# Kernel tuning notes

Hardware: AMD Instinct MI355X
Metric: run time of the kernel (lower is better)

## Reference

```python
import jax, jax.numpy as jnp
import numpy as np

DIM, HEADS, DIM_HEAD = 1024, 16, 64
DIM_INNER = HEADS * DIM_HEAD  # 1024
SCALE = DIM_HEAD ** -0.5


def _rope(t):
    # t: [b, h, n, d]; interleaved-pair RoPE (lucidrains rotary-embedding-torch default)
    d = t.shape[-1]
    n = t.shape[-2]
    inv_freq = 1.0 / (10000.0 ** (jnp.arange(0, d, 2, dtype=jnp.float32) / d))
    angles = jnp.arange(n, dtype=jnp.float32)[:, None] * inv_freq[None, :]  # [n, d/2]
    cos, sin = jnp.cos(angles), jnp.sin(angles)
    t1, t2 = t[..., 0::2], t[..., 1::2]
    r1 = t1 * cos - t2 * sin
    r2 = t1 * sin + t2 * cos
    return jnp.stack([r1, r2], axis=-1).reshape(t.shape)


def setup_inputs() -> dict:
    key = jax.random.key(0)
    ks = jax.random.split(key, 8)
    b, n = 2, 2048
    inp = {
        "x": jax.random.normal(ks[0], (b, n, DIM), dtype=jnp.float32),
        "value_residual": jax.random.normal(ks[1], (b, HEADS, n, DIM_HEAD), dtype=jnp.float32),
        "gamma": jnp.ones((DIM,), dtype=jnp.float32),
        "w_qkv": jax.random.normal(ks[2], (DIM, 3 * DIM_INNER), dtype=jnp.float32) * (DIM ** -0.5),
        "w_mix": jax.random.normal(ks[3], (DIM, HEADS), dtype=jnp.float32) * (DIM ** -0.5),
        "b_mix": jnp.zeros((HEADS,), dtype=jnp.float32),
        "w_gates": jax.random.normal(ks[4], (DIM, HEADS), dtype=jnp.float32) * (DIM ** -0.5),
        "b_gates": jnp.zeros((HEADS,), dtype=jnp.float32),
        "w_out": jax.random.normal(ks[5], (DIM_INNER, DIM), dtype=jnp.float32) * (DIM_INNER ** -0.5),
    }
    return inp


def reference(x, value_residual, gamma, w_qkv, w_mix, b_mix, w_gates, b_gates, w_out):
    b, n, _ = x.shape
    # RMSNorm (lucidrains style: F.normalize * sqrt(dim) * gamma)
    norm = jnp.sqrt(jnp.sum(x * x, axis=-1, keepdims=True))
    xn = x / jnp.maximum(norm, 1e-12) * (DIM ** 0.5) * gamma

    qkv = xn @ w_qkv  # [b, n, 3*h*d]
    qkv = qkv.reshape(b, n, 3, HEADS, DIM_HEAD)
    q, k, v = [jnp.transpose(qkv[:, :, i], (0, 2, 1, 3)) for i in range(3)]  # [b,h,n,d]
    original_values = v

    # learned value-residual lerp
    mix = jax.nn.sigmoid(xn @ w_mix + b_mix)            # [b, n, h]
    mix = jnp.transpose(mix, (0, 2, 1))[..., None]       # [b, h, n, 1]
    v = v * (1.0 - mix) + value_residual * mix

    # rotary on q, k
    q = _rope(q)
    k = _rope(k)

    scores = jnp.einsum("bhid,bhjd->bhij", q, k) * SCALE
    attn = jax.nn.softmax(scores, axis=-1)
    out = jnp.einsum("bhij,bhjd->bhid", attn, v)         # [b, h, n, d]

    gates = jax.nn.sigmoid(xn @ w_gates + b_gates)       # [b, n, h]
    out = out * jnp.transpose(gates, (0, 2, 1))[..., None]

    out = jnp.transpose(out, (0, 2, 1, 3)).reshape(b, n, DIM_INNER)
    return out @ w_out, original_values
```

## Files before the change

### kernel.cpp

```cpp
#include <hip/hip_runtime.h>
#include <hip/hip_bf16.h>
#include <math.h>

#define DIMSZ 1024
#define HEADS 16
#define DHEAD 64
#define NSEQ  2048
#define BATCH 2
#define ROWS  (BATCH*NSEQ)
#define SCALE 0.125f
#define LOG2E 1.4426950408889634f

typedef __attribute__((ext_vector_type(8))) short short8;
typedef __attribute__((ext_vector_type(4))) float floatx4;
typedef __attribute__((ext_vector_type(16))) float floatx16;
typedef __attribute__((ext_vector_type(4))) unsigned uintx4;

#define MFMA16(a,b,c) __builtin_amdgcn_mfma_f32_16x16x32_bf16(a,b,c,0,0,0)
#define MFMA32(a,b,c) __builtin_amdgcn_mfma_f32_32x32x16_bf16(a,b,c,0,0,0)

__device__ __forceinline__ void gl2lds16(const void* g, void* l) {
    __builtin_amdgcn_global_load_lds(
        (const __attribute__((address_space(1))) unsigned int*)g,
        (__attribute__((address_space(3))) unsigned int*)l, 16, 0, 0);
}

__device__ __forceinline__ unsigned short bf16r(float a) {
    unsigned u = __float_as_uint(a);
    u += 0x7fff + ((u >> 16) & 1);
    return (unsigned short)(u >> 16);
}
__device__ __forceinline__ unsigned pack_bf16(float a, float b) {
    unsigned ua = __float_as_uint(a), ub = __float_as_uint(b);
    ua += 0x7fff + ((ua >> 16) & 1);
    ub += 0x7fff + ((ub >> 16) & 1);
    return (ua >> 16) | (ub & 0xffff0000u);
}
__device__ __forceinline__ float2 bf2f(unsigned u) {
    float2 r;
    r.x = __uint_as_float(u << 16);
    r.y = __uint_as_float(u & 0xffff0000u);
    return r;
}
__device__ __forceinline__ unsigned cvtpk(float lo, float hi) {
    unsigned r;
    asm("v_cvt_pk_bf16_f32 %0, %1, %2" : "=v"(r) : "v"(lo), "v"(hi));
    return r;
}
__device__ __forceinline__ void pl32swap(unsigned &a, unsigned &b) {
#if __has_builtin(__builtin_amdgcn_permlane32_swap)
    auto r = __builtin_amdgcn_permlane32_swap(a, b, false, false);
    a = (unsigned)r[0]; b = (unsigned)r[1];
#else
    asm volatile("v_permlane32_swap_b32 %0, %1" : "+v"(a), "+v"(b));
#endif
}
__device__ __forceinline__ float fexp2(float x) {
#if __has_builtin(__builtin_amdgcn_exp2f)
    return __builtin_amdgcn_exp2f(x);
#else
    return exp2f(x);
#endif
}
__device__ __forceinline__ float fsin_rev(float x) {
#if __has_builtin(__builtin_amdgcn_sinf)
    return __builtin_amdgcn_sinf(x);
#else
    return __sinf(x * 6.28318530717958647692f);
#endif
}
__device__ __forceinline__ float fcos_rev(float x) {
#if __has_builtin(__builtin_amdgcn_cosf)
    return __builtin_amdgcn_cosf(x);
#else
    return __cosf(x * 6.28318530717958647692f);
#endif
}

#define SWZ(row) (((row) & 7) ^ (((row) >> 3) & 1))

__global__ __launch_bounds__(256) void transpose_all_kernel(
    const float* __restrict__ w_qkv, const float* __restrict__ w_out,
    const float* __restrict__ w_mix, const float* __restrict__ w_gates,
    unsigned short* __restrict__ wqkvT, unsigned short* __restrict__ woutT,
    unsigned short* __restrict__ wmgT, float* __restrict__ rtab)
{
    __shared__ float t[32][33];
    const int tx = threadIdx.x & 31, tyy = threadIdx.x >> 5;
    const int bx = blockIdx.x;
    const int k0 = blockIdx.y * 32;
    if (bx < 128) {
        const float* src;
        unsigned short* dst;
        int N, n0;
        if (bx < 96) { src = w_qkv; dst = wqkvT; N = 3*DIMSZ; n0 = bx*32; }
        else         { src = w_out; dst = woutT; N = DIMSZ;   n0 = (bx-96)*32; }
        #pragma unroll
        for (int i = 0; i < 4; i++)
            t[tyy*4 + i][tx] = src[(size_t)(k0 + tyy*4 + i)*N + n0 + tx];
        __syncthreads();
        #pragma unroll
        for (int i = 0; i < 4; i++)
            dst[(size_t)(n0 + tyy*4 + i)*DIMSZ + k0 + tx] = bf16r(t[tx][tyy*4 + i]);
    } else if (bx == 128) {
        #pragma unroll
        for (int i = 0; i < 4; i++) {
            const int kk = k0 + tyy*4 + i;
            t[tyy*4 + i][tx] = (tx < 16) ? w_mix[kk*16 + tx]
                                         : w_gates[kk*16 + (tx - 16)];
        }
        __syncthreads();
        #pragma unroll
        for (int i = 0; i < 4; i++)
            wmgT[(size_t)(tyy*4 + i)*DIMSZ + k0 + tx] = bf16r(t[tx][tyy*4 + i]);
    } else {
        const int pos = blockIdx.y*64 + (threadIdx.x >> 2);
        const int f0 = (threadIdx.x & 3) * 8;
        float2* dst = (float2*)rtab + (size_t)pos*32 + f0;
        #pragma unroll
        for (int tt = 0; tt < 8; tt++) {
            const float pf = (float)(f0 + tt);
            const float rev = (float)pos * fexp2(-pf * 0.41524101186092029f
                                                 - 2.6514961294723187f);
            const float rf = rev - floorf(rev);
            float2 cs;
            cs.x = fcos_rev(rf);
            cs.y = fsin_rev(rf);
            dst[tt] = cs;
        }
    }
}

__global__ __launch_bounds__(256) void rmsnorm_kernel(
    const float* __restrict__ x, const float* __restrict__ gamma,
    unsigned short* __restrict__ xnb)
{
    const int row = blockIdx.x;
    const int tid = threadIdx.x;
    __shared__ float wred[4];

    const float4 xv = ((const float4*)(x + (size_t)row * DIMSZ))[tid];
    float ss = xv.x*xv.x + xv.y*xv.y + xv.z*xv.z + xv.w*xv.w;
    #pragma unroll
    for (int off = 1; off < 64; off <<= 1) ss += __shfl_xor(ss, off);
    if ((tid & 63) == 0) wred[tid >> 6] = ss;
    __syncthreads();
    const float total = wred[0] + wred[1] + wred[2] + wred[3];
    const float inv = 32.0f / fmaxf(sqrtf(total), 1e-12f);
    const float4 gv = ((const float4*)gamma)[tid];
    uint2 pk;
    pk.x = pack_bf16(xv.x * inv * gv.x, xv.y * inv * gv.y);
    pk.y = pack_bf16(xv.z * inv * gv.z, xv.w * inv * gv.w);
    ((uint2*)(xnb + (size_t)row * DIMSZ))[tid] = pk;
}

__global__ __launch_bounds__(256) void mix_gates_mfma(
    const unsigned short* __restrict__ A, const unsigned short* __restrict__ WG,
    const float* __restrict__ b_mix, const float* __restrict__ b_gates,
    float* __restrict__ mixo, float* __restrict__ gateso)
{
    __shared__ short As[128*32];
    __shared__ short Bs[32*32];
    const int tid = threadIdx.x;
    const int wv = tid >> 6, lane = tid & 63;
    const int g = lane >> 4, c = lane & 15;
    const int bm = blockIdx.x * 128;

    floatx4 acc[2][2];
    #pragma unroll
    for (int mt = 0; mt < 2; mt++)
        #pragma unroll
        for (int nt = 0; nt < 2; nt++) acc[mt][nt] = (floatx4){0.f,0.f,0.f,0.f};

    for (int k0 = 0; k0 < DIMSZ; k0 += 32) {
        __syncthreads();
        #pragma unroll
        for (int r = 0; r < 2; r++) {
            const int ch = tid + 256*r;
            const int row = ch >> 2, cc = ch & 3;
            gl2lds16(A + (size_t)(bm + row)*DIMSZ + k0 + cc*8, (void*)(As + ch*8));
        }
        if (tid < 128)
            gl2lds16(WG + (size_t)(tid >> 2)*DIMSZ + k0 + (tid & 3)*8, (void*)(Bs + tid*8));
        __syncthreads();
        short8 af[2], bf[2];
        #pragma unroll
        for (int mt = 0; mt < 2; mt++) af[mt] = *(const short8*)(As + (wv*32 + mt*16 + c)*32 + g*8);
        #pragma unroll
        for (int nt = 0; nt < 2; nt++) bf[nt] = *(const short8*)(Bs + (nt*16 + c)*32 + g*8);
        #pragma unroll
        for (int mt = 0; mt < 2; mt++)
            #pragma unroll
            for (int nt = 0; nt < 2; nt++)
                acc[mt][nt] = MFMA16(af[mt], bf[nt], acc[mt][nt]);
    }
    const float bm_c = b_mix[c], bg_c = b_gates[c];
    #pragma unroll
    for (int mt = 0; mt < 2; mt++)
        #pragma unroll
        for (int r2 = 0; r2 < 4; r2++) {
            const int row = bm + wv*32 + mt*16 + g*4 + r2;
            const float lm = acc[mt][0][r2] + bm_c;
            const float lg = acc[mt][1][r2] + bg_c;
            mixo[(size_t)row*HEADS + c]   = 1.0f / (1.0f + fexp2(-lm * LOG2E));
            gateso[(size_t)row*HEADS + c] = 1.0f / (1.0f + fexp2(-lg * LOG2E));
        }
}

__device__ __forceinline__ void stage_qkv(
    const unsigned short* A, const unsigned short* BT,
    short* as, short* bs, int bm, int bn, int kk, int tid)
{
    #pragma unroll
    for (int r = 0; r < 2; r++) {
        const int ch = tid + 256*r;
        const int row = ch >> 2, j = ch & 3;
        gl2lds16(A  + (size_t)(bm + row)*DIMSZ + kk + j*8, (void*)(as + ch*8));
        gl2lds16(BT + (size_t)(bn + row)*DIMSZ + kk + j*8, (void*)(bs + ch*8));
    }
}

__global__ __launch_bounds__(256) void gemm_qkv_mfma(
    const unsigned short* __restrict__ A, const unsigned short* __restrict__ BT,
    unsigned short* __restrict__ qb, unsigned short* __restrict__ kb,
    float* __restrict__ vb)
{
    __shared__ short As[3][128*32];
    __shared__ short Bs[3][128*32];
    const int tid = threadIdx.x;
    const int wv = tid >> 6, lane = tid & 63;
    const int g = lane >> 4, c = lane & 15;
    const int wm = wv >> 1, wn = wv & 1;

    const int id = blockIdx.y * gridDim.x + blockIdx.x;
    const int xcd = id & 7, j = id >> 3;
    const int bnb = (xcd & 1)*12 + (j % 12);
    const int byb = (xcd >> 1)*8 + (j / 12);
    const int bm = byb * 128, bn = bnb * 128;

    floatx4 acc[4][4];
    #pragma unroll
    for (int mt = 0; mt < 4; mt++)
        #pragma unroll
        for (int nt = 0; nt < 4; nt++) acc[mt][nt] = (floatx4){0.f,0.f,0.f,0.f};

    stage_qkv(A, BT, &As[0][0], &Bs[0][0], bm, bn, 0,  tid);
    stage_qkv(A, BT, &As[1][0], &Bs[1][0], bm, bn, 32, tid);
    asm volatile("s_waitcnt vmcnt(4)" ::: "memory");
    __builtin_amdgcn_s_barrier();
    __builtin_amdgcn_sched_barrier(0);

    int cur = 0, nxt = 2;
    for (int i = 0; i < 32; i++) {
        const int k0 = i*32;
        if (i < 30)
            stage_qkv(A, BT, &As[nxt][0], &Bs[nxt][0], bm, bn, k0 + 64, tid);

        short8 af[4], bf[4];
        #pragma unroll
        for (int mt = 0; mt < 4; mt++) af[mt] = *(const short8*)(&As[cur][0] + (wm*64 + mt*16 + c)*32 + g*8);
        #pragma unroll
        for (int nt = 0; nt < 4; nt++) bf[nt] = *(const short8*)(&Bs[cur][0] + (wn*64 + nt*16 + c)*32 + g*8);
        __builtin_amdgcn_s_setprio(1);
        #pragma unroll
        for (int mt = 0; mt < 4; mt++)
            #pragma unroll
            for (int nt = 0; nt < 4; nt++)
                acc[mt][nt] = MFMA16(af[mt], bf[nt], acc[mt][nt]);
        __builtin_amdgcn_s_setprio(0);

        if (i < 31) {
            if (i < 30) asm volatile("s_waitcnt vmcnt(4)" ::: "memory");
            else        asm volatile("s_waitcnt vmcnt(0)" ::: "memory");
            __builtin_amdgcn_s_barrier();
            __builtin_amdgcn_sched_barrier(0);
        }
        cur = (cur == 2) ? 0 : cur + 1;
        nxt = (nxt == 2) ? 0 : nxt + 1;
    }
    __syncthreads();

    const int i3 = bn >> 10;
    const int nb = bn - (i3 << 10);
    if (i3 < 2) {
        unsigned short* dst = (i3 == 0) ? qb : kb;
        short* wbuf = &As[0][0] + wv*1152;
        const int rd_row = lane >> 2, seg = lane & 3;
        #pragma unroll
        for (int mt = 0; mt < 4; mt++) {
            #pragma unroll
            for (int nt = 0; nt < 4; nt++)
                #pragma unroll
                for (int r2 = 0; r2 < 4; r2++)
                    wbuf[(g*4 + r2)*72 + nt*16 + c] = (short)bf16r(acc[mt][nt][r2]);
            __builtin_amdgcn_s_waitcnt(0xc07f);
            const uint4 v0 = *(const uint4*)&wbuf[rd_row*72 + seg*16];
            const uint4 v1 = *(const uint4*)&wbuf[rd_row*72 + seg*16 + 8];
            const int row = bm + wm*64 + mt*16 + rd_row;
            const int col = nb + wn*64 + seg*16;
            const int hh = col >> 6, dd = col & 63;
            const int bb2 = row >> 11, pos = row & 2047;
            unsigned short* dp = dst + (((size_t)(bb2*HEADS + hh)*NSEQ) + pos)*DHEAD + dd;
            *(uint4*)dp = v0;
            *(uint4*)(dp + 8) = v1;
            __builtin_amdgcn_s_waitcnt(0xc07f);
        }
    } else {
        #pragma unroll
        for (int mt = 0; mt < 4; mt++)
            #pragma unroll
            for (int nt = 0; nt < 4; nt++)
                #pragma unroll
                for (int r2 = 0; r2 < 4; r2++) {
                    const int row = bm + wm*64 + mt*16 + g*4 + r2;
                    const int col = nb + wn*64 + nt*16 + c;
                    const int hh = col >> 6, dd = col & 63;
                    const int bb2 = row >> 11, pos = row & 2047;
                    vb[(((size_t)(bb2*HEADS + hh)*NSEQ) + pos)*DHEAD + dd] = acc[mt][nt][r2];
                }
    }
}

__global__ __launch_bounds__(256) void rope_blend_kernel2(
    unsigned short* __restrict__ q, unsigned short* __restrict__ k,
    const float* __restrict__ vorig, const float* __restrict__ vres,
    const float* __restrict__ mixb, const float* __restrict__ rtab,
    unsigned short* __restrict__ vT)
{
    __shared__ unsigned short vt[64*72];
    const int tid = threadIdx.x;
    const int bh = blockIdx.y, bb = bh >> 4, h = bh & 15;
    const int p0 = blockIdx.x * 64;
    {
        const int pr = tid >> 2, d0 = (tid & 3) * 16;
        const int pos = p0 + pr;
        const size_t base = ((size_t)bh*NSEQ + pos)*DHEAD + d0;

        float cs_sn[16];
        #pragma unroll
        for (int i = 0; i < 4; i++)
            *(float4*)(cs_sn + i*4) = *(const float4*)(rtab + (size_t)pos*64 + d0 + i*4);

        uint4 qr0 = *(uint4*)(q + base), qr1 = *(uint4*)(q + base + 8);
        uint4 kr0 = *(uint4*)(k + base), kr1 = *(uint4*)(k + base + 8);
        unsigned qw[8] = {qr0.x, qr0.y, qr0.z, qr0.w, qr1.x, qr1.y, qr1.z, qr1.w};
        unsigned kw[8] = {kr0.x, kr0.y, kr0.z, kr0.w, kr1.x, kr1.y, kr1.z, kr1.w};
        const float QSC = SCALE * LOG2E;
        #pragma unroll
        for (int j = 0; j < 8; j++) {
            const float cs = cs_sn[2*j], sn = cs_sn[2*j + 1];
            float2 qv = bf2f(qw[j]);
            float2 kv = bf2f(kw[j]);
            const float q1 = qv.x*cs - qv.y*sn, q2 = qv.x*sn + qv.y*cs;
            const float k1 = kv.x*cs - kv.y*sn, k2 = kv.x*sn + kv.y*cs;
            qw[j] = pack_bf16(q1*QSC, q2*QSC);
            kw[j] = pack_bf16(k1, k2);
        }
        *(uint4*)(q + base)     = *(uint4*)(qw + 0);
        *(uint4*)(q + base + 8) = *(uint4*)(qw + 4);
        *(uint4*)(k + base)     = *(uint4*)(kw + 0);
        *(uint4*)(k + base + 8) = *(uint4*)(kw + 4);

        float vv[16], vr[16];
        #pragma unroll
        for (int i = 0; i < 4; i++) {
            *(float4*)(vv + i*4) = *(const float4*)(vorig + base + i*4);
            *(float4*)(vr + i*4) = *(const float4*)(vres + base + i*4);
        }
        const float mx = mixb[((size_t)(bb*NSEQ + pos))*HEADS + h];
        #pragma unroll
        for (int j = 0; j < 8; j++) {
            const float b0 = vv[2*j]*(1.f-mx)   + vr[2*j]*mx;
            const float b1 = vv[2*j+1]*(1.f-mx) + vr[2*j+1]*mx;
            vt[pr*72 + d0 + 2*j]     = bf16r(b0);
            vt[pr*72 + d0 + 2*j + 1] = bf16r(b1);
        }
    }
    __syncthreads();
    {
        const int dd = tid >> 2, c0 = (tid & 3) * 16;
        unsigned o[8];
        #pragma unroll
        for (int j = 0; j < 8; j++) {
            const unsigned a  = vt[(c0 + 2*j)*72 + dd];
            const unsigned b2 = vt[(c0 + 2*j + 1)*72 + dd];
            o[j] = a | (b2 << 16);
        }
        unsigned short* dst = vT + ((size_t)bh*DHEAD + dd)*NSEQ + p0 + c0;
        *(uint4*)(dst)     = *(uint4*)(o + 0);
        *(uint4*)(dst + 8) = *(uint4*)(o + 4);
    }
}

__global__ __launch_bounds__(256, 4) void attn_mfma_kernel(
    const unsigned short* __restrict__ qg,
    const unsigned short* __restrict__ kg,
    const unsigned short* __restrict__ vT,
    unsigned short* __restrict__ Op0,
    unsigned short* __restrict__ Op1,
    float* __restrict__ lpart)
{
    __shared__ short Kt[2][64*64];
    __shared__ short Vt[2][64*64];

    const int tid = threadIdx.x;
    const int w = tid >> 6, lane = tid & 63;
    const int hi = lane >> 5, cq = lane & 31;

    int wg = blockIdx.y * gridDim.x + blockIdx.x;
    wg = (wg & 7) * 128 + (wg >> 3);
    const int q0 = (wg & 15) * 128;
    const int byy = wg >> 4;
    const int bh = byy >> 1, s = byy & 1;
    const int bb = bh >> 4, h = bh & 15;

    short8 qf[4];
    #pragma unroll
    for (int kd = 0; kd < 4; kd++)
        qf[kd] = *(const short8*)(qg + ((size_t)bh*NSEQ + q0 + w*32 + cq)*DHEAD + kd*16 + hi*8);

    floatx16 O0{}, O1{};
    float lsum = 0.f;

    const unsigned short* kbase = kg + (size_t)bh*NSEQ*DHEAD;
    const unsigned short* vbase = vT + (size_t)bh*DHEAD*NSEQ;

    {
        const int kt = s*16;
        #pragma unroll
        for (int r = 0; r < 2; r++) {
            const int ch = tid + 256*r;
            const int row = ch >> 3;
            const int u = (ch & 7) ^ SWZ(row);
            gl2lds16(kbase + (size_t)(kt*64 + row)*DHEAD + u*8, (void*)(&Kt[0][0] + ch*8));
            gl2lds16(vbase + (size_t)row*NSEQ + kt*64 + u*8,   (void*)(&Vt[0][0] + ch*8));
        }
    }
    __syncthreads();

    for (int i = 0; i < 16; i++) {
        const int cur = i & 1;
        const short* Ktc = &Kt[cur][0];
        const short* Vtc = &Vt[cur][0];

        if (i < 15) {
            const int kt = s*16 + i + 1;
            short* Ktn = &Kt[cur ^ 1][0];
            short* Vtn = &Vt[cur ^ 1][0];
            #pragma unroll
            for (int r = 0; r < 2; r++) {
                const int ch = tid + 256*r;
                const int row = ch >> 3;
                const int u = (ch & 7) ^ SWZ(row);
                gl2lds16(kbase + (size_t)(kt*64 + row)*DHEAD + u*8, (void*)(Ktn + ch*8));
                gl2lds16(vbase + (size_t)row*NSEQ + kt*64 + u*8,   (void*)(Vtn + ch*8));
            }
        }

        floatx16 accS0{}, accS1{};
        __builtin_amdgcn_s_setprio(1);
        #pragma unroll
        for (int kd = 0; kd < 4; kd++) {
            const int r0 = cq, r1 = 32 + cq;
            short8 kf0 = *(const short8*)(Ktc + r0*64 + (((kd*2 + hi) ^ SWZ(r0)) * 8));
            short8 kf1 = *(const short8*)(Ktc + r1*64 + (((kd*2 + hi) ^ SWZ(r1)) * 8));
            accS0 = MFMA32(kf0, qf[kd], accS0);
            accS1 = MFMA32(kf1, qf[kd], accS1);
        }
        __builtin_amdgcn_s_setprio(0);

        #pragma unroll
        for (int kt2 = 0; kt2 < 2; kt2++) {
            const floatx16 accS = kt2 ? accS1 : accS0;

            float p[16];
            #pragma unroll
            for (int r = 0; r < 16; r++) p[r] = fexp2(accS[r]);
            const float a1 = (p[0]+p[1]) + (p[2]+p[3]);
            const float a2 = (p[4]+p[5]) + (p[6]+p[7]);
            const float a3 = (p[8]+p[9]) + (p[10]+p[11]);
            const float a4 = (p[12]+p[13]) + (p[14]+p[15]);
            lsum += (a1+a2) + (a3+a4);

            unsigned d0 = cvtpk(p[0],  p[1]);
            unsigned d1 = cvtpk(p[2],  p[3]);
            unsigned d2 = cvtpk(p[4],  p[5]);
            unsigned d3 = cvtpk(p[6],  p[7]);
            unsigned d4 = cvtpk(p[8],  p[9]);
            unsigned d5 = cvtpk(p[10], p[11]);
            unsigned d6 = cvtpk(p[12], p[13]);
            unsigned d7 = cvtpk(p[14], p[15]);
            pl32swap(d0, d2);
            pl32swap(d1, d3);
            pl32swap(d4, d6);
            pl32swap(d5, d7);
            const uintx4 t0 = {d0, d1, d2, d3};
            const uintx4 t1 = {d4, d5, d6, d7};
            const short8 pf0 = __builtin_bit_cast(short8, t0);
            const short8 pf1 = __builtin_bit_cast(short8, t1);

            __builtin_amdgcn_s_setprio(1);
            #pragma unroll
            for (int ks2 = 0; ks2 < 2; ks2++) {
                const short8 pf = ks2 ? pf1 : pf0;
                #pragma unroll
                for (int nt2 = 0; nt2 < 2; nt2++) {
                    const int rv = nt2*32 + cq;
                    short8 vf = *(const short8*)(Vtc + rv*64 + (((kt2*4 + ks2*2 + hi) ^ SWZ(rv)) * 8));
                    if (nt2 == 0) O0 = MFMA32(pf, vf, O0);
                    else          O1 = MFMA32(pf, vf, O1);
                }
            }
            __builtin_amdgcn_s_setprio(0);
        }
        __syncthreads();
    }

    unsigned short* Op = s ? Op1 : Op0;
    float l = lsum + __shfl_xor(lsum, 32);
    if (hi == 0)
        lpart[((size_t)s*ROWS + bb*NSEQ + q0 + w*32 + cq)*HEADS + h] = l;
    #pragma unroll
    for (int reg = 0; reg < 16; reg++) {
        const int qq = (reg & 3) + 8*(reg >> 2) + 4*hi;
        const int rowg = q0 + w*32 + qq;
        unsigned short* op = Op + ((size_t)(bb*NSEQ + rowg))*DIMSZ + h*DHEAD + cq;
        op[0]  = bf16r(O0[reg]);
        op[32] = bf16r(O1[reg]);
    }
}

__global__ __launch_bounds__(256) void attn_combine_kernel(
    const unsigned short* __restrict__ Op1, const float* __restrict__ lpart,
    const float* __restrict__ gates, unsigned short* __restrict__ attnO)
{
    const int idx = blockIdx.x * 256 + threadIdx.x;
    const int row = idx >> 7;
    const int c8 = (idx & 127) * 8;
    const int h = c8 >> 6;
    const float l0 = lpart[(size_t)row*HEADS + h];
    const float l1 = lpart[((size_t)ROWS + row)*HEADS + h];
    const float gt = gates[(size_t)row*HEADS + h];
    const float sc = gt / (l0 + l1);
    const size_t base = (size_t)row*DIMSZ + c8;
    const uint4 a = *(const uint4*)(attnO + base);
    const uint4 b = *(const uint4*)(Op1 + base);
    const unsigned aw[4] = {a.x, a.y, a.z, a.w};
    const unsigned bw[4] = {b.x, b.y, b.z, b.w};
    unsigned o[4];
    #pragma unroll
    for (int j = 0; j < 4; j++) {
        const float2 fa = bf2f(aw[j]);
        const float2 fb = bf2f(bw[j]);
        o[j] = pack_bf16((fa.x + fb.x)*sc, (fa.y + fb.y)*sc);
    }
    *(uint4*)(attnO + base) = *(uint4*)o;
}

__device__ __forceinline__ void stage_out(
    const unsigned short* A, const unsigned short* BT,
    short* as, short* bs, int bm, int bn, int kk, int tid)
{
    #pragma unroll
    for (int r = 0; r < 2; r++) {
        const int ch = tid + 256*r;
        const int row = ch >> 2, j = ch & 3;
        gl2lds16(A + (size_t)(bm + row)*DIMSZ + kk + j*8, (void*)(as + ch*8));
    }
    gl2lds16(BT + (size_t)(bn + (tid >> 2))*DIMSZ + kk + (tid & 3)*8, (void*)(bs + tid*8));
}

__global__ __launch_bounds__(256) void gemm_out_mfma(
    const unsigned short* __restrict__ A, const unsigned short* __restrict__ BT,
    float* __restrict__ out0)
{
    __shared__ short As[3][128*32];
    __shared__ short Bs[3][64*32];
    const int tid = threadIdx.x;
    const int wv = tid >> 6, lane = tid & 63;
    const int g = lane >> 4, c = lane & 15;
    const int wm = wv >> 1, wn = wv & 1;

    const int id = blockIdx.y * gridDim.x + blockIdx.x;
    const int xcd = id & 7, j = id >> 3;
    const int bnb = j & 15, byb = xcd*4 + (j >> 4);
    const int bm = byb * 128, bn = bnb * 64;

    floatx4 acc[4][2];
    #pragma unroll
    for (int mt = 0; mt < 4; mt++)
        #pragma unroll
        for (int nt = 0; nt < 2; nt++) acc[mt][nt] = (floatx4){0.f,0.f,0.f,0.f};

    stage_out(A, BT, &As[0][0], &Bs[0][0], bm, bn, 0,  tid);
    stage_out(A, BT, &As[1][0], &Bs[1][0], bm, bn, 32, tid);
    asm volatile("s_waitcnt vmcnt(3)" ::: "memory");
    __builtin_amdgcn_s_barrier();
    __builtin_amdgcn_sched_barrier(0);

    int cur = 0, nxt = 2;
    for (int i = 0; i < 32; i++) {
        const int k0 = i*32;
        if (i < 30)
            stage_out(A, BT, &As[nxt][0], &Bs[nxt][0], bm, bn, k0 + 64, tid);

        short8 af[4], bf[2];
        #pragma unroll
        for (int mt = 0; mt < 4; mt++) af[mt] = *(const short8*)(&As[cur][0] + (wm*64 + mt*16 + c)*32 + g*8);
        #pragma unroll
        for (int nt = 0; nt < 2; nt++) bf[nt] = *(const short8*)(&Bs[cur][0] + (wn*32 + nt*16 + c)*32 + g*8);
        __builtin_amdgcn_s_setprio(1);
        #pragma unroll
        for (int mt = 0; mt < 4; mt++)
            #pragma unroll
            for (int nt = 0; nt < 2; nt++)
                acc[mt][nt] = MFMA16(af[mt], bf[nt], acc[mt][nt]);
        __builtin_amdgcn_s_setprio(0);

        if (i < 31) {
            if (i < 30) asm volatile("s_waitcnt vmcnt(3)" ::: "memory");
            else        asm volatile("s_waitcnt vmcnt(0)" ::: "memory");
            __builtin_amdgcn_s_barrier();
            __builtin_amdgcn_sched_barrier(0);
        }
        cur = (cur == 2) ? 0 : cur + 1;
        nxt = (nxt == 2) ? 0 : nxt + 1;
    }

    #pragma unroll
    for (int mt = 0; mt < 4; mt++)
        #pragma unroll
        for (int nt = 0; nt < 2; nt++)
            #pragma unroll
            for (int r2 = 0; r2 < 4; r2++) {
                const int row = bm + wm*64 + mt*16 + g*4 + r2;
                const int col = bn + wn*32 + nt*16 + c;
                out0[(size_t)row*DIMSZ + col] = acc[mt][nt][r2];
            }
}

extern "C" void kernel_launch(void* const* d_in, const int* in_sizes, int n_in,
                              void* d_out, int out_size, void* d_ws, size_t ws_size,
                              hipStream_t stream) {
    const float* x       = (const float*)d_in[0];
    const float* vres    = (const float*)d_in[1];
    const float* gamma   = (const float*)d_in[2];
    const float* w_qkv   = (const float*)d_in[3];
    const float* w_mix   = (const float*)d_in[4];
    const float* b_mix   = (const float*)d_in[5];
    const float* w_gates = (const float*)d_in[6];
    const float* b_gates = (const float*)d_in[7];
    const float* w_out   = (const float*)d_in[8];

    float* out0 = (float*)d_out;
    float* out1 = out0 + (size_t)ROWS * DIMSZ;

    char* ws = (char*)d_ws;
    unsigned short* xnb   = (unsigned short*)(ws);
    unsigned short* wqkvT = (unsigned short*)(ws + (8u<<20));
    unsigned short* woutT = (unsigned short*)(ws + (14u<<20));
    unsigned short* qb2   = (unsigned short*)(ws + (16u<<20));
    unsigned short* kb2   = (unsigned short*)(ws + (24u<<20));
    unsigned short* vT    = (unsigned short*)(ws + (32u<<20));
    unsigned short* attnO = (unsigned short*)(ws + (40u<<20));
    float*          mixb  = (float*)(ws + (48u<<20));
    float*          gatesb= (float*)(ws + (48u<<20) + 262144);
    unsigned short* wmgT  = (unsigned short*)(ws + (49u<<20));
    unsigned short* Op1   = (unsigned short*)(ws + (50u<<20));
    float*          lpart = (float*)(ws + (58u<<20));
    float*          rtab  = (float*)(ws + (59u<<20));

    transpose_all_kernel<<<dim3(130, DIMSZ/32), 256, 0, stream>>>(
        w_qkv, w_out, w_mix, w_gates, wqkvT, woutT, wmgT, rtab);

    rmsnorm_kernel<<<ROWS, 256, 0, stream>>>(x, gamma, xnb);

    mix_gates_mfma<<<ROWS/128, 256, 0, stream>>>(
        xnb, wmgT, b_mix, b_gates, mixb, gatesb);

    gemm_qkv_mfma<<<dim3(3*DIMSZ/128, ROWS/128), 256, 0, stream>>>(
        xnb, wqkvT, qb2, kb2, out1);

    rope_blend_kernel2<<<dim3(NSEQ/64, BATCH*HEADS), 256, 0, stream>>>(
        qb2, kb2, out1, vres, mixb, rtab, vT);

    attn_mfma_kernel<<<dim3(NSEQ/128, BATCH*HEADS*2), 256, 0, stream>>>(
        qb2, kb2, vT, attnO, Op1, lpart);

    attn_combine_kernel<<<ROWS*DIMSZ/8/256, 256, 0, stream>>>(
        Op1, lpart, gatesb, attnO);

    gemm_out_mfma<<<dim3(DIMSZ/64, ROWS/128), 256, 0, stream>>>(
        attnO, woutT, out0);
}
```

Before: 237.2 us.

## Use BK=64 double-buffered swizzled LDS tiles in QKV and output GEMMs

Both bf16 MFMA GEMMs move from a 3-stage pipeline with 32-wide K tiles to a 2-stage pipeline with 64-wide K tiles. Halving the main-loop iterations halves the barriers, and LDS rows are XOR-swizzled (SWZ) to avoid bank conflicts on the wider row stride. The catch is the prefetch schedule: the next tile is now issued only after compute on the current buffer finishes, so load/compute overlap is shallower and LDS use grows.

After: 242.4 us. 2.2% more time.

```diff
diff --git a/kernel.cpp b/kernel.cpp
--- a/kernel.cpp
+++ b/kernel.cpp
@@ -212,11 +212,12 @@
     short* as, short* bs, int bm, int bn, int kk, int tid)
 {
     #pragma unroll
-    for (int r = 0; r < 2; r++) {
+    for (int r = 0; r < 4; r++) {
         const int ch = tid + 256*r;
-        const int row = ch >> 2, j = ch & 3;
-        gl2lds16(A  + (size_t)(bm + row)*DIMSZ + kk + j*8, (void*)(as + ch*8));
-        gl2lds16(BT + (size_t)(bn + row)*DIMSZ + kk + j*8, (void*)(bs + ch*8));
+        const int row = ch >> 3;
+        const int u = (ch & 7) ^ SWZ(row);
+        gl2lds16(A  + (size_t)(bm + row)*DIMSZ + kk + u*8, (void*)(as + ch*8));
+        gl2lds16(BT + (size_t)(bn + row)*DIMSZ + kk + u*8, (void*)(bs + ch*8));
     }
 }
 
@@ -225,8 +226,8 @@
     unsigned short* __restrict__ qb, unsigned short* __restrict__ kb,
     float* __restrict__ vb)
 {
-    __shared__ short As[3][128*32];
-    __shared__ short Bs[3][128*32];
+    __shared__ short As[2][128*64];
+    __shared__ short Bs[2][128*64];
     const int tid = threadIdx.x;
     const int wv = tid >> 6, lane = tid & 63;
     const int g = lane >> 4, c = lane & 15;
@@ -245,38 +246,47 @@
         for (int nt = 0; nt < 4; nt++) acc[mt][nt] = (floatx4){0.f,0.f,0.f,0.f};
 
     stage_qkv(A, BT, &As[0][0], &Bs[0][0], bm, bn, 0,  tid);
-    stage_qkv(A, BT, &As[1][0], &Bs[1][0], bm, bn, 32, tid);
-    asm volatile("s_waitcnt vmcnt(4)" ::: "memory");
+    stage_qkv(A, BT, &As[1][0], &Bs[1][0], bm, bn, 64, tid);
+    asm volatile("s_waitcnt vmcnt(8)" ::: "memory");
     __builtin_amdgcn_s_barrier();
     __builtin_amdgcn_sched_barrier(0);
 
-    int cur = 0, nxt = 2;
-    for (int i = 0; i < 32; i++) {
-        const int k0 = i*32;
-        if (i < 30)
-            stage_qkv(A, BT, &As[nxt][0], &Bs[nxt][0], bm, bn, k0 + 64, tid);
-
-        short8 af[4], bf[4];
-        #pragma unroll
-        for (int mt = 0; mt < 4; mt++) af[mt] = *(const short8*)(&As[cur][0] + (wm*64 + mt*16 + c)*32 + g*8);
-        #pragma unroll
-        for (int nt = 0; nt < 4; nt++) bf[nt] = *(const short8*)(&Bs[cur][0] + (wn*64 + nt*16 + c)*32 + g*8);
-        __builtin_amdgcn_s_setprio(1);
-        #pragma unroll
-        for (int mt = 0; mt < 4; mt++)
-            #pragma unroll
-            for (int nt = 0; nt < 4; nt++)
-                acc[mt][nt] = MFMA16(af[mt], bf[nt], acc[mt][nt]);
-        __builtin_amdgcn_s_setprio(0);
-
-        if (i < 31) {
-            if (i < 30) asm volatile("s_waitcnt vmcnt(4)" ::: "memory");
-            else        asm volatile("s_waitcnt vmcnt(0)" ::: "memory");
+    for (int i = 0; i < 16; i++) {
+        const int cur = i & 1;
+        const short* Ac = &As[cur][0];
+        const short* Bc = &Bs[cur][0];
+        #pragma unroll
+        for (int kb = 0; kb < 2; kb++) {
+            short8 af[4], bf[4];
+            #pragma unroll
+            for (int mt = 0; mt < 4; mt++) {
+                const int row = wm*64 + mt*16 + c;
+                af[mt] = *(const short8*)(Ac + row*64 + (((kb*4 + g) ^ SWZ(row)) * 8));
+            }
+            #pragma unroll
+            for (int nt = 0; nt < 4; nt++) {
+                const int row = wn*64 + nt*16 + c;
+                bf[nt] = *(const short8*)(Bc + row*64 + (((kb*4 + g) ^ SWZ(row)) * 8));
+            }
+            __builtin_amdgcn_s_setprio(1);
+            #pragma unroll
+            for (int mt = 0; mt < 4; mt++)
+                #pragma unroll
+                for (int nt = 0; nt < 4; nt++)
+                    acc[mt][nt] = MFMA16(af[mt], bf[nt], acc[mt][nt]);
+            __builtin_amdgcn_s_setprio(0);
+        }
+        __builtin_amdgcn_s_barrier();
+        if (i < 14) {
+            stage_qkv(A, BT, &As[cur][0], &Bs[cur][0], bm, bn, (i + 2)*64, tid);
+            asm volatile("s_waitcnt vmcnt(8)" ::: "memory");
             __builtin_amdgcn_s_barrier();
             __builtin_amdgcn_sched_barrier(0);
-        }
-        cur = (cur == 2) ? 0 : cur + 1;
-        nxt = (nxt == 2) ? 0 : nxt + 1;
+        } else if (i == 14) {
+            asm volatile("s_waitcnt vmcnt(0)" ::: "memory");
+            __builtin_amdgcn_s_barrier();
+            __builtin_amdgcn_sched_barrier(0);
+        }
     }
     __syncthreads();
 
@@ -562,20 +572,27 @@
     short* as, short* bs, int bm, int bn, int kk, int tid)
 {
     #pragma unroll
+    for (int r = 0; r < 4; r++) {
+        const int ch = tid + 256*r;
+        const int row = ch >> 3;
+        const int u = (ch & 7) ^ SWZ(row);
+        gl2lds16(A + (size_t)(bm + row)*DIMSZ + kk + u*8, (void*)(as + ch*8));
+    }
+    #pragma unroll
     for (int r = 0; r < 2; r++) {
         const int ch = tid + 256*r;
-        const int row = ch >> 2, j = ch & 3;
-        gl2lds16(A + (size_t)(bm + row)*DIMSZ + kk + j*8, (void*)(as + ch*8));
-    }
-    gl2lds16(BT + (size_t)(bn + (tid >> 2))*DIMSZ + kk + (tid & 3)*8, (void*)(bs + tid*8));
+        const int row = ch >> 3;
+        const int u = (ch & 7) ^ SWZ(row);
+        gl2lds16(BT + (size_t)(bn + row)*DIMSZ + kk + u*8, (void*)(bs + ch*8));
+    }
 }
 
 __global__ __launch_bounds__(256) void gemm_out_mfma(
     const unsigned short* __restrict__ A, const unsigned short* __restrict__ BT,
     float* __restrict__ out0)
 {
-    __shared__ short As[3][128*32];
-    __shared__ short Bs[3][64*32];
+    __shared__ short As[2][128*64];
+    __shared__ short Bs[2][64*64];
     const int tid = threadIdx.x;
     const int wv = tid >> 6, lane = tid & 63;
     const int g = lane >> 4, c = lane & 15;
@@ -593,38 +610,47 @@
         for (int nt = 0; nt < 2; nt++) acc[mt][nt] = (floatx4){0.f,0.f,0.f,0.f};
 
     stage_out(A, BT, &As[0][0], &Bs[0][0], bm, bn, 0,  tid);
-    stage_out(A, BT, &As[1][0], &Bs[1][0], bm, bn, 32, tid);
-    asm volatile("s_waitcnt vmcnt(3)" ::: "memory");
+    stage_out(A, BT, &As[1][0], &Bs[1][0], bm, bn, 64, tid);
+    asm volatile("s_waitcnt vmcnt(6)" ::: "memory");
     __builtin_amdgcn_s_barrier();
     __builtin_amdgcn_sched_barrier(0);
 
-    int cur = 0, nxt = 2;
-    for (int i = 0; i < 32; i++) {
-        const int k0 = i*32;
-        if (i < 30)
-            stage_out(A, BT, &As[nxt][0], &Bs[nxt][0], bm, bn, k0 + 64, tid);
-
-        short8 af[4], bf[2];
-        #pragma unroll
-        for (int mt = 0; mt < 4; mt++) af[mt] = *(const short8*)(&As[cur][0] + (wm*64 + mt*16 + c)*32 + g*8);
-        #pragma unroll
-        for (int nt = 0; nt < 2; nt++) bf[nt] = *(const short8*)(&Bs[cur][0] + (wn*32 + nt*16 + c)*32 + g*8);
-        __builtin_amdgcn_s_setprio(1);
-        #pragma unroll
-        for (int mt = 0; mt < 4; mt++)
-            #pragma unroll
-            for (int nt = 0; nt < 2; nt++)
-                acc[mt][nt] = MFMA16(af[mt], bf[nt], acc[mt][nt]);
-        __builtin_amdgcn_s_setprio(0);
-
-        if (i < 31) {
-            if (i < 30) asm volatile("s_waitcnt vmcnt(3)" ::: "memory");
-            else        asm volatile("s_waitcnt vmcnt(0)" ::: "memory");
+    for (int i = 0; i < 16; i++) {
+        const int cur = i & 1;
+        const short* Ac = &As[cur][0];
+        const short* Bc = &Bs[cur][0];
+        #pragma unroll
+        for (int kb = 0; kb < 2; kb++) {
+            short8 af[4], bf[2];
+            #pragma unroll
+            for (int mt = 0; mt < 4; mt++) {
+                const int row = wm*64 + mt*16 + c;
+                af[mt] = *(const short8*)(Ac + row*64 + (((kb*4 + g) ^ SWZ(row)) * 8));
+            }
+            #pragma unroll
+            for (int nt = 0; nt < 2; nt++) {
+                const int row = wn*32 + nt*16 + c;
+                bf[nt] = *(const short8*)(Bc + row*64 + (((kb*4 + g) ^ SWZ(row)) * 8));
+            }
+            __builtin_amdgcn_s_setprio(1);
+            #pragma unroll
+            for (int mt = 0; mt < 4; mt++)
+                #pragma unroll
+                for (int nt = 0; nt < 2; nt++)
+                    acc[mt][nt] = MFMA16(af[mt], bf[nt], acc[mt][nt]);
+            __builtin_amdgcn_s_setprio(0);
+        }
+        __builtin_amdgcn_s_barrier();
+        if (i < 14) {
+            stage_out(A, BT, &As[cur][0], &Bs[cur][0], bm, bn, (i + 2)*64, tid);
+            asm volatile("s_waitcnt vmcnt(6)" ::: "memory");
             __builtin_amdgcn_s_barrier();
             __builtin_amdgcn_sched_barrier(0);
-        }
-        cur = (cur == 2) ? 0 : cur + 1;
-        nxt = (nxt == 2) ? 0 : nxt + 1;
+        } else if (i == 14) {
+            asm volatile("s_waitcnt vmcnt(0)" ::: "memory");
+            __builtin_amdgcn_s_barrier();
+            __builtin_amdgcn_sched_barrier(0);
+        }
     }
 
     #pragma unroll
```

## Drop split-KV attention, fuse normalization and gating into attention epilogue

Applied to the files above, without the earlier changes.

Attention no longer splits the key sequence into two halves. Each workgroup now walks all 32 KV tiles and applies the softmax normalization and sigmoid gate in its epilogue, which removes the combine kernel, the partial-output buffers and the lpart traffic. Separately, the RMSNorm and weight-transpose/rope-table kernels are merged into one launch. The cost is half as many attention workgroups (512 instead of 1024), each doing twice the serial work, which lowers parallelism and latency hiding.

New measurement: 231.5 us. 1.02x faster.

```diff
diff --git a/kernel.cpp b/kernel.cpp
--- a/kernel.cpp
+++ b/kernel.cpp
@@ -79,16 +79,41 @@
 
 #define SWZ(row) (((row) & 7) ^ (((row) >> 3) & 1))
 
-__global__ __launch_bounds__(256) void transpose_all_kernel(
+__global__ __launch_bounds__(256) void prep_kernel(
+    const float* __restrict__ x, const float* __restrict__ gamma,
     const float* __restrict__ w_qkv, const float* __restrict__ w_out,
     const float* __restrict__ w_mix, const float* __restrict__ w_gates,
+    unsigned short* __restrict__ xnb,
     unsigned short* __restrict__ wqkvT, unsigned short* __restrict__ woutT,
     unsigned short* __restrict__ wmgT, float* __restrict__ rtab)
 {
     __shared__ float t[32][33];
-    const int tx = threadIdx.x & 31, tyy = threadIdx.x >> 5;
-    const int bx = blockIdx.x;
-    const int k0 = blockIdx.y * 32;
+    __shared__ float wred[4];
+    const int bid = blockIdx.x;
+    const int tid = threadIdx.x;
+
+    if (bid < ROWS) {
+        const int row = bid;
+        const float4 xv = ((const float4*)(x + (size_t)row * DIMSZ))[tid];
+        float ss = xv.x*xv.x + xv.y*xv.y + xv.z*xv.z + xv.w*xv.w;
+        #pragma unroll
+        for (int off = 1; off < 64; off <<= 1) ss += __shfl_xor(ss, off);
+        if ((tid & 63) == 0) wred[tid >> 6] = ss;
+        __syncthreads();
+        const float total = wred[0] + wred[1] + wred[2] + wred[3];
+        const float inv = 32.0f / fmaxf(sqrtf(total), 1e-12f);
+        const float4 gv = ((const float4*)gamma)[tid];
+        uint2 pk;
+        pk.x = pack_bf16(xv.x * inv * gv.x, xv.y * inv * gv.y);
+        pk.y = pack_bf16(xv.z * inv * gv.z, xv.w * inv * gv.w);
+        ((uint2*)(xnb + (size_t)row * DIMSZ))[tid] = pk;
+        return;
+    }
+
+    const int tb = bid - ROWS;
+    const int bx = tb % 130;
+    const int k0 = (tb / 130) * 32;
+    const int tx = tid & 31, tyy = tid >> 5;
     if (bx < 128) {
         const float* src;
         unsigned short* dst;
@@ -114,8 +139,8 @@
         for (int i = 0; i < 4; i++)
             wmgT[(size_t)(tyy*4 + i)*DIMSZ + k0 + tx] = bf16r(t[tx][tyy*4 + i]);
     } else {
-        const int pos = blockIdx.y*64 + (threadIdx.x >> 2);
-        const int f0 = (threadIdx.x & 3) * 8;
+        const int pos = (k0 >> 5)*64 + (tid >> 2);
+        const int f0 = (tid & 3) * 8;
         float2* dst = (float2*)rtab + (size_t)pos*32 + f0;
         #pragma unroll
         for (int tt = 0; tt < 8; tt++) {
@@ -129,29 +154,6 @@
             dst[tt] = cs;
         }
     }
-}
-
-__global__ __launch_bounds__(256) void rmsnorm_kernel(
-    const float* __restrict__ x, const float* __restrict__ gamma,
-    unsigned short* __restrict__ xnb)
-{
-    const int row = blockIdx.x;
-    const int tid = threadIdx.x;
-    __shared__ float wred[4];
-
-    const float4 xv = ((const float4*)(x + (size_t)row * DIMSZ))[tid];
-    float ss = xv.x*xv.x + xv.y*xv.y + xv.z*xv.z + xv.w*xv.w;
-    #pragma unroll
-    for (int off = 1; off < 64; off <<= 1) ss += __shfl_xor(ss, off);
-    if ((tid & 63) == 0) wred[tid >> 6] = ss;
-    __syncthreads();
-    const float total = wred[0] + wred[1] + wred[2] + wred[3];
-    const float inv = 32.0f / fmaxf(sqrtf(total), 1e-12f);
-    const float4 gv = ((const float4*)gamma)[tid];
-    uint2 pk;
-    pk.x = pack_bf16(xv.x * inv * gv.x, xv.y * inv * gv.y);
-    pk.y = pack_bf16(xv.z * inv * gv.z, xv.w * inv * gv.w);
-    ((uint2*)(xnb + (size_t)row * DIMSZ))[tid] = pk;
 }
 
 __global__ __launch_bounds__(256) void mix_gates_mfma(
@@ -396,22 +398,21 @@
     const unsigned short* __restrict__ qg,
     const unsigned short* __restrict__ kg,
     const unsigned short* __restrict__ vT,
-    unsigned short* __restrict__ Op0,
-    unsigned short* __restrict__ Op1,
-    float* __restrict__ lpart)
+    const float* __restrict__ gates,
+    unsigned short* __restrict__ attnO)
 {
     __shared__ short Kt[2][64*64];
     __shared__ short Vt[2][64*64];
+    __shared__ float lred[4][32];
 
     const int tid = threadIdx.x;
     const int w = tid >> 6, lane = tid & 63;
     const int hi = lane >> 5, cq = lane & 31;
 
     int wg = blockIdx.y * gridDim.x + blockIdx.x;
-    wg = (wg & 7) * 128 + (wg >> 3);
+    wg = (wg & 7) * 64 + (wg >> 3);
     const int q0 = (wg & 15) * 128;
-    const int byy = wg >> 4;
-    const int bh = byy >> 1, s = byy & 1;
+    const int bh = wg >> 4;
     const int bb = bh >> 4, h = bh & 15;
 
     short8 qf[4];
@@ -425,26 +426,23 @@
     const unsigned short* kbase = kg + (size_t)bh*NSEQ*DHEAD;
     const unsigned short* vbase = vT + (size_t)bh*DHEAD*NSEQ;
 
-    {
-        const int kt = s*16;
-        #pragma unroll
-        for (int r = 0; r < 2; r++) {
-            const int ch = tid + 256*r;
-            const int row = ch >> 3;
-            const int u = (ch & 7) ^ SWZ(row);
-            gl2lds16(kbase + (size_t)(kt*64 + row)*DHEAD + u*8, (void*)(&Kt[0][0] + ch*8));
-            gl2lds16(vbase + (size_t)row*NSEQ + kt*64 + u*8,   (void*)(&Vt[0][0] + ch*8));
-        }
+    #pragma unroll
+    for (int r = 0; r < 2; r++) {
+        const int ch = tid + 256*r;
+        const int row = ch >> 3;
+        const int u = (ch & 7) ^ SWZ(row);
+        gl2lds16(kbase + (size_t)row*DHEAD + u*8, (void*)(&Kt[0][0] + ch*8));
+        gl2lds16(vbase + (size_t)row*NSEQ + u*8,  (void*)(&Vt[0][0] + ch*8));
     }
     __syncthreads();
 
-    for (int i = 0; i < 16; i++) {
+    for (int i = 0; i < 32; i++) {
         const int cur = i & 1;
         const short* Ktc = &Kt[cur][0];
         const short* Vtc = &Vt[cur][0];
 
-        if (i < 15) {
-            const int kt = s*16 + i + 1;
+        if (i < 31) {
+            const int kt = i + 1;
             short* Ktn = &Kt[cur ^ 1][0];
             short* Vtn = &Vt[cur ^ 1][0];
             #pragma unroll
@@ -516,45 +514,19 @@
         __syncthreads();
     }
 
-    unsigned short* Op = s ? Op1 : Op0;
     float l = lsum + __shfl_xor(lsum, 32);
-    if (hi == 0)
-        lpart[((size_t)s*ROWS + bb*NSEQ + q0 + w*32 + cq)*HEADS + h] = l;
+    if (hi == 0) lred[w][cq] = l;
+    __builtin_amdgcn_s_waitcnt(0xc07f);
     #pragma unroll
     for (int reg = 0; reg < 16; reg++) {
         const int qq = (reg & 3) + 8*(reg >> 2) + 4*hi;
         const int rowg = q0 + w*32 + qq;
-        unsigned short* op = Op + ((size_t)(bb*NSEQ + rowg))*DIMSZ + h*DHEAD + cq;
-        op[0]  = bf16r(O0[reg]);
-        op[32] = bf16r(O1[reg]);
-    }
-}
-
-__global__ __launch_bounds__(256) void attn_combine_kernel(
-    const unsigned short* __restrict__ Op1, const float* __restrict__ lpart,
-    const float* __restrict__ gates, unsigned short* __restrict__ attnO)
-{
-    const int idx = blockIdx.x * 256 + threadIdx.x;
-    const int row = idx >> 7;
-    const int c8 = (idx & 127) * 8;
-    const int h = c8 >> 6;
-    const float l0 = lpart[(size_t)row*HEADS + h];
-    const float l1 = lpart[((size_t)ROWS + row)*HEADS + h];
-    const float gt = gates[(size_t)row*HEADS + h];
-    const float sc = gt / (l0 + l1);
-    const size_t base = (size_t)row*DIMSZ + c8;
-    const uint4 a = *(const uint4*)(attnO + base);
-    const uint4 b = *(const uint4*)(Op1 + base);
-    const unsigned aw[4] = {a.x, a.y, a.z, a.w};
-    const unsigned bw[4] = {b.x, b.y, b.z, b.w};
-    unsigned o[4];
-    #pragma unroll
-    for (int j = 0; j < 4; j++) {
-        const float2 fa = bf2f(aw[j]);
-        const float2 fb = bf2f(bw[j]);
-        o[j] = pack_bf16((fa.x + fb.x)*sc, (fa.y + fb.y)*sc);
-    }
-    *(uint4*)(attnO + base) = *(uint4*)o;
+        const float gt = gates[((size_t)(bb*NSEQ + rowg))*HEADS + h];
+        const float sc = gt / lred[w][qq];
+        unsigned short* op = attnO + ((size_t)(bb*NSEQ + rowg))*DIMSZ + h*DHEAD + cq;
+        op[0]  = bf16r(O0[reg] * sc);
+        op[32] = bf16r(O1[reg] * sc);
+    }
 }
 
 __device__ __forceinline__ void stage_out(
@@ -666,14 +638,10 @@
     float*          mixb  = (float*)(ws + (48u<<20));
     float*          gatesb= (float*)(ws + (48u<<20) + 262144);
     unsigned short* wmgT  = (unsigned short*)(ws + (49u<<20));
-    unsigned short* Op1   = (unsigned short*)(ws + (50u<<20));
-    float*          lpart = (float*)(ws + (58u<<20));
     float*          rtab  = (float*)(ws + (59u<<20));
 
-    transpose_all_kernel<<<dim3(130, DIMSZ/32), 256, 0, stream>>>(
-        w_qkv, w_out, w_mix, w_gates, wqkvT, woutT, wmgT, rtab);
-
-    rmsnorm_kernel<<<ROWS, 256, 0, stream>>>(x, gamma, xnb);
+    prep_kernel<<<ROWS + 130*(DIMSZ/32), 256, 0, stream>>>(
+        x, gamma, w_qkv, w_out, w_mix, w_gates, xnb, wqkvT, woutT, wmgT, rtab);
 
     mix_gates_mfma<<<ROWS/128, 256, 0, stream>>>(
         xnb, wmgT, b_mix, b_gates, mixb, gatesb);
@@ -684,11 +652,8 @@
     rope_blend_kernel2<<<dim3(NSEQ/64, BATCH*HEADS), 256, 0, stream>>>(
         qb2, kb2, out1, vres, mixb, rtab, vT);
 
-    attn_mfma_kernel<<<dim3(NSEQ/128, BATCH*HEADS*2), 256, 0, stream>>>(
-        qb2, kb2, vT, attnO, Op1, lpart);
-
-    attn_combine_kernel<<<ROWS*DIMSZ/8/256, 256, 0, stream>>>(
-        Op1, lpart, gatesb, attnO);
+    attn_mfma_kernel<<<dim3(NSEQ/128, BATCH*HEADS), 256, 0, stream>>>(
+        qb2, kb2, vT, gatesb, attnO);
 
     gemm_out_mfma<<<dim3(DIMSZ/64, ROWS/128), 256, 0, stream>>>(
         attnO, woutT, out0);
```

## Merge rmsnorm into weight-prep kernel and split-K the mix/gates GEMM

Applied to the files above, without the earlier changes.

Folds the RMSNorm kernel into the weight transpose/rope-table kernel as extra blocks, removing one launch and letting the two independent jobs share the GPU. The mix/gates projection now uses 32-row tiles, with each wave owning a quarter of K. Each wave double-buffers its own LDS stages, and the partial sums are reduced through shared memory. This gives four times as many blocks and no block-wide barriers in the K loop, at the cost of more LDS and a final reduction.

Result: faster. 229.5 us (-3.3%).

```diff
diff --git a/kernel.cpp b/kernel.cpp
--- a/kernel.cpp
+++ b/kernel.cpp
@@ -79,16 +79,41 @@
 
 #define SWZ(row) (((row) & 7) ^ (((row) >> 3) & 1))
 
-__global__ __launch_bounds__(256) void transpose_all_kernel(
+__global__ __launch_bounds__(256) void prep_kernel(
+    const float* __restrict__ x, const float* __restrict__ gamma,
     const float* __restrict__ w_qkv, const float* __restrict__ w_out,
     const float* __restrict__ w_mix, const float* __restrict__ w_gates,
+    unsigned short* __restrict__ xnb,
     unsigned short* __restrict__ wqkvT, unsigned short* __restrict__ woutT,
     unsigned short* __restrict__ wmgT, float* __restrict__ rtab)
 {
     __shared__ float t[32][33];
-    const int tx = threadIdx.x & 31, tyy = threadIdx.x >> 5;
-    const int bx = blockIdx.x;
-    const int k0 = blockIdx.y * 32;
+    __shared__ float wred[4];
+    const int bid = blockIdx.x;
+    const int tid = threadIdx.x;
+
+    if (bid < ROWS) {
+        const int row = bid;
+        const float4 xv = ((const float4*)(x + (size_t)row * DIMSZ))[tid];
+        float ss = xv.x*xv.x + xv.y*xv.y + xv.z*xv.z + xv.w*xv.w;
+        #pragma unroll
+        for (int off = 1; off < 64; off <<= 1) ss += __shfl_xor(ss, off);
+        if ((tid & 63) == 0) wred[tid >> 6] = ss;
+        __syncthreads();
+        const float total = wred[0] + wred[1] + wred[2] + wred[3];
+        const float inv = 32.0f / fmaxf(sqrtf(total), 1e-12f);
+        const float4 gv = ((const float4*)gamma)[tid];
+        uint2 pk;
+        pk.x = pack_bf16(xv.x * inv * gv.x, xv.y * inv * gv.y);
+        pk.y = pack_bf16(xv.z * inv * gv.z, xv.w * inv * gv.w);
+        ((uint2*)(xnb + (size_t)row * DIMSZ))[tid] = pk;
+        return;
+    }
+
+    const int tb = bid - ROWS;
+    const int bx = tb % 130;
+    const int k0 = (tb / 130) * 32;
+    const int tx = tid & 31, tyy = tid >> 5;
     if (bx < 128) {
         const float* src;
         unsigned short* dst;
@@ -114,8 +139,8 @@
         for (int i = 0; i < 4; i++)
             wmgT[(size_t)(tyy*4 + i)*DIMSZ + k0 + tx] = bf16r(t[tx][tyy*4 + i]);
     } else {
-        const int pos = blockIdx.y*64 + (threadIdx.x >> 2);
-        const int f0 = (threadIdx.x & 3) * 8;
+        const int pos = (k0 >> 5)*64 + (tid >> 2);
+        const int f0 = (tid & 3) * 8;
         float2* dst = (float2*)rtab + (size_t)pos*32 + f0;
         #pragma unroll
         for (int tt = 0; tt < 8; tt++) {
@@ -131,40 +156,19 @@
     }
 }
 
-__global__ __launch_bounds__(256) void rmsnorm_kernel(
-    const float* __restrict__ x, const float* __restrict__ gamma,
-    unsigned short* __restrict__ xnb)
-{
-    const int row = blockIdx.x;
-    const int tid = threadIdx.x;
-    __shared__ float wred[4];
-
-    const float4 xv = ((const float4*)(x + (size_t)row * DIMSZ))[tid];
-    float ss = xv.x*xv.x + xv.y*xv.y + xv.z*xv.z + xv.w*xv.w;
-    #pragma unroll
-    for (int off = 1; off < 64; off <<= 1) ss += __shfl_xor(ss, off);
-    if ((tid & 63) == 0) wred[tid >> 6] = ss;
-    __syncthreads();
-    const float total = wred[0] + wred[1] + wred[2] + wred[3];
-    const float inv = 32.0f / fmaxf(sqrtf(total), 1e-12f);
-    const float4 gv = ((const float4*)gamma)[tid];
-    uint2 pk;
-    pk.x = pack_bf16(xv.x * inv * gv.x, xv.y * inv * gv.y);
-    pk.y = pack_bf16(xv.z * inv * gv.z, xv.w * inv * gv.w);
-    ((uint2*)(xnb + (size_t)row * DIMSZ))[tid] = pk;
-}
-
 __global__ __launch_bounds__(256) void mix_gates_mfma(
     const unsigned short* __restrict__ A, const unsigned short* __restrict__ WG,
     const float* __restrict__ b_mix, const float* __restrict__ b_gates,
     float* __restrict__ mixo, float* __restrict__ gateso)
 {
-    __shared__ short As[128*32];
-    __shared__ short Bs[32*32];
+    __shared__ short As[4][2][32*32];
+    __shared__ short Bs[4][2][32*32];
+    __shared__ float red[4][32*32];
     const int tid = threadIdx.x;
     const int wv = tid >> 6, lane = tid & 63;
     const int g = lane >> 4, c = lane & 15;
-    const int bm = blockIdx.x * 128;
+    const int bm = blockIdx.x * 32;
+    const int kbase = wv * 256;
 
     floatx4 acc[2][2];
     #pragma unroll
@@ -172,39 +176,61 @@
         #pragma unroll
         for (int nt = 0; nt < 2; nt++) acc[mt][nt] = (floatx4){0.f,0.f,0.f,0.f};
 
-    for (int k0 = 0; k0 < DIMSZ; k0 += 32) {
-        __syncthreads();
-        #pragma unroll
-        for (int r = 0; r < 2; r++) {
-            const int ch = tid + 256*r;
-            const int row = ch >> 2, cc = ch & 3;
-            gl2lds16(A + (size_t)(bm + row)*DIMSZ + k0 + cc*8, (void*)(As + ch*8));
-        }
-        if (tid < 128)
-            gl2lds16(WG + (size_t)(tid >> 2)*DIMSZ + k0 + (tid & 3)*8, (void*)(Bs + tid*8));
-        __syncthreads();
+    #pragma unroll
+    for (int r = 0; r < 2; r++) {
+        const int ch = lane + 64*r;
+        const int row = ch >> 2, cc = ch & 3;
+        gl2lds16(A  + (size_t)(bm + row)*DIMSZ + kbase + cc*8, (void*)(&As[wv][0][0] + ch*8));
+        gl2lds16(WG + (size_t)row*DIMSZ        + kbase + cc*8, (void*)(&Bs[wv][0][0] + ch*8));
+    }
+    for (int i = 0; i < 8; i++) {
+        const int cur = i & 1;
+        if (i < 7) {
+            const int k0 = kbase + (i + 1)*32;
+            #pragma unroll
+            for (int r = 0; r < 2; r++) {
+                const int ch = lane + 64*r;
+                const int row = ch >> 2, cc = ch & 3;
+                gl2lds16(A  + (size_t)(bm + row)*DIMSZ + k0 + cc*8, (void*)(&As[wv][cur^1][0] + ch*8));
+                gl2lds16(WG + (size_t)row*DIMSZ        + k0 + cc*8, (void*)(&Bs[wv][cur^1][0] + ch*8));
+            }
+            asm volatile("s_waitcnt vmcnt(4)" ::: "memory");
+        } else {
+            asm volatile("s_waitcnt vmcnt(0)" ::: "memory");
+        }
+        __builtin_amdgcn_sched_barrier(0);
         short8 af[2], bf[2];
         #pragma unroll
-        for (int mt = 0; mt < 2; mt++) af[mt] = *(const short8*)(As + (wv*32 + mt*16 + c)*32 + g*8);
-        #pragma unroll
-        for (int nt = 0; nt < 2; nt++) bf[nt] = *(const short8*)(Bs + (nt*16 + c)*32 + g*8);
+        for (int mt = 0; mt < 2; mt++) af[mt] = *(const short8*)(&As[wv][cur][0] + (mt*16 + c)*32 + g*8);
+        #pragma unroll
+        for (int nt = 0; nt < 2; nt++) bf[nt] = *(const short8*)(&Bs[wv][cur][0] + (nt*16 + c)*32 + g*8);
         #pragma unroll
         for (int mt = 0; mt < 2; mt++)
             #pragma unroll
             for (int nt = 0; nt < 2; nt++)
                 acc[mt][nt] = MFMA16(af[mt], bf[nt], acc[mt][nt]);
     }
-    const float bm_c = b_mix[c], bg_c = b_gates[c];
     #pragma unroll
     for (int mt = 0; mt < 2; mt++)
         #pragma unroll
-        for (int r2 = 0; r2 < 4; r2++) {
-            const int row = bm + wv*32 + mt*16 + g*4 + r2;
-            const float lm = acc[mt][0][r2] + bm_c;
-            const float lg = acc[mt][1][r2] + bg_c;
-            mixo[(size_t)row*HEADS + c]   = 1.0f / (1.0f + fexp2(-lm * LOG2E));
-            gateso[(size_t)row*HEADS + c] = 1.0f / (1.0f + fexp2(-lg * LOG2E));
-        }
+        for (int nt = 0; nt < 2; nt++)
+            #pragma unroll
+            for (int r2 = 0; r2 < 4; r2++)
+                red[wv][(mt*16 + g*4 + r2)*32 + nt*16 + c] = acc[mt][nt][r2];
+    __syncthreads();
+    #pragma unroll
+    for (int jj = 0; jj < 4; jj++) {
+        const int idx = tid + jj*256;
+        const int row = idx >> 5, col = idx & 31;
+        const float s = (red[0][idx] + red[1][idx]) + (red[2][idx] + red[3][idx]);
+        if (col < 16) {
+            const float lm = s + b_mix[col];
+            mixo[(size_t)(bm + row)*HEADS + col] = 1.0f / (1.0f + fexp2(-lm * LOG2E));
+        } else {
+            const float lg = s + b_gates[col - 16];
+            gateso[(size_t)(bm + row)*HEADS + (col - 16)] = 1.0f / (1.0f + fexp2(-lg * LOG2E));
+        }
+    }
 }
 
 __device__ __forceinline__ void stage_qkv(
@@ -670,12 +696,10 @@
     float*          lpart = (float*)(ws + (58u<<20));
     float*          rtab  = (float*)(ws + (59u<<20));
 
-    transpose_all_kernel<<<dim3(130, DIMSZ/32), 256, 0, stream>>>(
-        w_qkv, w_out, w_mix, w_gates, wqkvT, woutT, wmgT, rtab);
-
-    rmsnorm_kernel<<<ROWS, 256, 0, stream>>>(x, gamma, xnb);
-
-    mix_gates_mfma<<<ROWS/128, 256, 0, stream>>>(
+    prep_kernel<<<ROWS + 130*(DIMSZ/32), 256, 0, stream>>>(
+        x, gamma, w_qkv, w_out, w_mix, w_gates, xnb, wqkvT, woutT, wmgT, rtab);
+
+    mix_gates_mfma<<<ROWS/32, 256, 0, stream>>>(
         xnb, wmgT, b_mix, b_gates, mixb, gatesb);
 
     gemm_qkv_mfma<<<dim3(3*DIMSZ/128, ROWS/128), 256, 0, stream>>>(
```
